# Performance work log

Measured on AMD Instinct MI355X. Metric: run time of the kernel, lower is better.

## Reference

```python
import jax, jax.numpy as jnp
import numpy as np

B, S, D, H = 2, 2048, 1024, 16
DK = D // H


def setup_inputs() -> dict:
    key = jax.random.key(0)
    ks = jax.random.split(key, 9)
    w_scale = 1.0 / np.sqrt(D)  # xavier-ish scale
    return {
        "q": jax.random.normal(ks[0], (B, S, D), dtype=jnp.float32),
        "k": jax.random.normal(ks[1], (B, S, D), dtype=jnp.float32),
        "v": jax.random.normal(ks[2], (B, S, D), dtype=jnp.float32),
        "A": jax.random.uniform(ks[3], (S, S), dtype=jnp.float32),
        "Wq": jax.random.normal(ks[4], (D, D), dtype=jnp.float32) * w_scale,
        "bq": jnp.zeros((D,), jnp.float32),
        "Wk": jax.random.normal(ks[5], (D, D), dtype=jnp.float32) * w_scale,
        "bk": jnp.zeros((D,), jnp.float32),
        "Wv": jax.random.normal(ks[6], (D, D), dtype=jnp.float32) * w_scale,
        "bv": jnp.zeros((D,), jnp.float32),
        "Wo": jax.random.normal(ks[7], (D, D), dtype=jnp.float32) * w_scale,
        "bo": jnp.zeros((D,), jnp.float32),
    }


def _proj(x, W, b):
    # nn.Linear: x @ W^T + b, then split heads -> [B, H, S, DK]
    y = jnp.einsum("bsd,ed->bse", x, W) + b
    return y.reshape(B, S, H, DK).transpose(0, 2, 1, 3)


def reference(q, k, v, A, Wq, bq, Wk, bk, Wv, bv, Wo, bo):
    qh = _proj(q, Wq, bq)  # [B,H,S,DK]
    kh = _proj(k, Wk, bk)
    vh = _proj(v, Wv, bv)
    scale = 1.0 / jnp.sqrt(jnp.asarray(DK, qh.dtype))
    scores = jnp.einsum("bhqd,bhkd->bhqk", qh, kh) * scale  # [B,H,S,S]
    # No softmax: scores multiplied by structural mask A^T (dropout disabled, eval)
    p_attn = scores * A.T
    x = jnp.einsum("bhqk,bhkd->bhqd", p_attn, vh)
    x = x.transpose(0, 2, 1, 3).reshape(B, S, D)
    return jnp.einsum("bsd,ed->bse", x, Wo) + bo
```

## Files before the change

kernel.cpp:

```cpp
#include <hip/hip_runtime.h>

#define SEQ    2048
#define DMODEL 1024
#define NHEAD  16
#define DHEAD  64
#define NBATCH 2

typedef __bf16 bf16x8 __attribute__((ext_vector_type(8)));
typedef float f32x16 __attribute__((ext_vector_type(16)));
typedef float f32x8 __attribute__((ext_vector_type(8)));
typedef unsigned short ushort8v __attribute__((ext_vector_type(8)));
typedef unsigned int uint2v __attribute__((ext_vector_type(2)));
typedef int int4v __attribute__((ext_vector_type(4)));

static __device__ __forceinline__ unsigned short f2b(float f){
  unsigned int u = __builtin_bit_cast(unsigned int, f);
  u += 0x7fffu + ((u>>16)&1u);
  return (unsigned short)(u>>16);
}
static __device__ __forceinline__ float b2f(unsigned short h){
  unsigned int u = ((unsigned int)h)<<16;
  return __builtin_bit_cast(float, u);
}
static __device__ __forceinline__ f32x16 mfma32(bf16x8 a, bf16x8 b, f32x16 c){
  return __builtin_amdgcn_mfma_f32_32x32x16_bf16(a,b,c,0,0,0);
}
static __device__ __forceinline__ ushort8v cvt8(const float* p){
  float4 f0 = *(const float4*)p;
  float4 f1 = *(const float4*)(p+4);
  ushort8v r;
  r[0]=f2b(f0.x); r[1]=f2b(f0.y); r[2]=f2b(f0.z); r[3]=f2b(f0.w);
  r[4]=f2b(f1.x); r[5]=f2b(f1.y); r[6]=f2b(f1.z); r[7]=f2b(f1.w);
  return r;
}
#define GLOAD16(g,l) __builtin_amdgcn_global_load_lds( \
    (const __attribute__((address_space(1))) void*)(g), \
    (__attribute__((address_space(3))) void*)(l), 16, 0, 0)

__global__ __launch_bounds__(256) void cvtXW(
    const float* __restrict__ q, const float* __restrict__ k, const float* __restrict__ v,
    const float* __restrict__ Wq, const float* __restrict__ Wk,
    const float* __restrict__ Wv, const float* __restrict__ Wo,
    unsigned short* __restrict__ Xq, unsigned short* __restrict__ Xk, unsigned short* __restrict__ Xv,
    unsigned short* __restrict__ Wp)
{
  const int z = blockIdx.z;
  const int wave = threadIdx.x>>6, lane = threadIdx.x&63;
  const int l31 = lane&31, hi = lane>>5;
  const float* S;
  unsigned short* dst;
  int g;
  if (z < 3){
    S = (z==0)? q : (z==1)? k : v;
    unsigned short* D = (z==0)? Xq : (z==1)? Xk : Xv;
    g = blockIdx.x;
    dst = D + (size_t)(g*64 + wave*16)*512 + lane*8;
  } else {
    const int wz = blockIdx.x>>5, gg = blockIdx.x&31;
    S = (wz==0)? Wq : (wz==1)? Wk : (wz==2)? Wv : Wo;
    g = gg;
    dst = Wp + (size_t)((wz*32 + gg)*64 + wave*16)*512 + lane*8;
  }
  const float* src = S + (size_t)(g*32 + l31)*DMODEL + 8*hi + 256*wave;
  #pragma unroll
  for (int i=0;i<16;i++)
    *(ushort8v*)(dst + (size_t)i*512) = cvt8(src + 16*i);
}

__global__ __launch_bounds__(256) void cvtA(const float* __restrict__ A,
                                            unsigned short* __restrict__ Am){
  const int tid  = threadIdx.x;
  const int lane = tid&63, l31 = lane&31, hi = lane>>5;
  const int q32  = blockIdx.x;
  const int kt   = blockIdx.y*4 + (tid>>6);
  const int q    = q32*32 + l31;

  unsigned short out8[4][8];
  #pragma unroll
  for (int fi=0; fi<2; fi++){
    #pragma unroll
    for (int mm=0; mm<4; mm++){
      #pragma unroll
      for (int j=0; j<4; j++){
        const int k = kt*64 + 32*fi + 8*mm + 4*hi + j;
        out8[fi*2 + (mm>>1)][(mm&1)*4 + j] = f2b(A[(size_t)k*SEQ + q]);
      }
    }
  }
  unsigned short* dst = Am + ((size_t)(q32*32 + kt)*4)*512 + lane*8;
  #pragma unroll
  for (int w=0; w<4; w++)
    *(ushort8v*)(dst + (size_t)w*512) = *(const ushort8v*)out8[w];
}

__global__ __launch_bounds__(256,3) void proj_qkv(
    const unsigned short* __restrict__ Xq, const unsigned short* __restrict__ Xk, const unsigned short* __restrict__ Xv,
    const unsigned short* __restrict__ Wp,
    const float* __restrict__ bq, const float* __restrict__ bk, const float* __restrict__ bv,
    unsigned short* __restrict__ qh, unsigned short* __restrict__ Kp, unsigned short* __restrict__ Vp)
{
  const int z = blockIdx.z;
  const unsigned short* X = (z==0)? Xq : (z==1)? Xk : Xv;
  const unsigned short* W = Wp + (size_t)z*1048576;
  const float* bias = (z==0)? bq : (z==1)? bk : bv;
  const float alpha = (z==0)? 0.125f : 1.0f;

  const int orig = blockIdx.y*8 + blockIdx.x;
  const int virt = (orig&7)*32 + (orig>>3);
  const int bx = virt&7, by = virt>>3;
  const int mb = by*128, nb = bx*128;

  const int tid = threadIdx.x;
  const int lane = tid&63, wave = tid>>6;
  const int wr = wave>>1, wc = wave&1, l31 = lane&31, hi = lane>>5;
  f32x16 acc[2][2] = {};

  const unsigned short* a0p = X + (size_t)((mb>>5) + 2*wr)*32768 + lane*8;
  const unsigned short* a1p = a0p + 32768;
  const unsigned short* b0p = W + (size_t)((nb>>5) + 2*wc)*32768 + lane*8;
  const unsigned short* b1p = b0p + 32768;

  #pragma unroll 8
  for (int s=0;s<64;s++){
    bf16x8 a0 = *(const bf16x8*)(a0p + (size_t)s*512);
    bf16x8 a1 = *(const bf16x8*)(a1p + (size_t)s*512);
    bf16x8 b0 = *(const bf16x8*)(b0p + (size_t)s*512);
    bf16x8 b1 = *(const bf16x8*)(b1p + (size_t)s*512);
    acc[0][0] = mfma32(a0,b0,acc[0][0]);
    acc[0][1] = mfma32(a0,b1,acc[0][1]);
    acc[1][0] = mfma32(a1,b0,acc[1][0]);
    acc[1][1] = mfma32(a1,b1,acc[1][1]);
  }

  #pragma unroll
  for (int fj=0; fj<2; fj++){
    const int e = nb + 64*wc + 32*fj + l31;
    const float bv_ = bias[e];
    const int hh = e>>6, dk = e&63;
    #pragma unroll
    for (int fi=0; fi<2; fi++){
      #pragma unroll
      for (int r=0;r<16;r++){
        const int i = mb + 64*wr + 32*fi + (r&3) + 8*(r>>2) + 4*hi;
        const int bb = i>>11, ss = i&(SEQ-1);
        const int bhh = bb*NHEAD + hh;
        const unsigned short val = f2b((acc[fi][fj][r] + bv_)*alpha);
        if (z==0){
          qh[((size_t)bhh*SEQ + ss)*DHEAD + dk] = val;
        } else if (z==1){
          const size_t addr = (((size_t)(bhh*64 + (ss>>5))*4 + (dk>>4))*64
                               + ((dk>>3)&1)*32 + (ss&31))*8 + (dk&7);
          Kp[addr] = val;
        } else {
          const size_t addr = ((((size_t)(bhh*32 + (ss>>6))*4 + ((ss>>4)&3))*2
                               + (dk>>5))*64 + ((ss>>3)&1)*32 + (dk&31))*8 + (ss&7);
          Vp[addr] = val;
        }
      }
    }
  }
}

__global__ __launch_bounds__(512,4) void attn(
    const unsigned short* __restrict__ qh, const unsigned short* __restrict__ Kp,
    const unsigned short* __restrict__ Vp, const unsigned short* __restrict__ Am,
    unsigned short* __restrict__ xp)
{
  const int orig = blockIdx.y*16 + blockIdx.x;
  const int xcd = orig&7, within = orig>>3;
  const int bh   = xcd*4 + (within>>4);
  const int qblk = within&15;

  const int tid  = threadIdx.x;
  const int lane = tid&63, wave = tid>>6;
  const int qsub = wave&3, khalf = wave>>2;
  const int l31 = lane&31, hi = lane>>5;

  const int q32  = qblk*4 + qsub;
  const int qrow = q32*32 + l31;
  const unsigned short* qp = qh + ((size_t)bh*SEQ + qrow)*DHEAD;
  bf16x8 Qf[4];
  #pragma unroll
  for (int t=0;t<4;t++) Qf[t] = *(const bf16x8*)(qp + 16*t + 8*hi);

  f32x16 xacc[2] = {};

  const unsigned short* kpb = Kp + (size_t)bh*131072 + lane*8;
  const unsigned short* vpb = Vp + (size_t)bh*131072 + lane*8;
  const unsigned short* apb = Am + (size_t)q32*65536 + lane*8;

  __shared__ float SMEMf[8448];
  unsigned short* smem = (unsigned short*)SMEMf;

  const unsigned short* gsb = ((wave<4)? kpb : vpb);
  const int fo = (wave&3)*2;
  const int dof = ((wave<4)? 0 : 4096) + fo*512;

  ushort8v Aa[2], Ab[2];

  #define STAGE(BUF, KT) { \
    const unsigned short* _g = gsb + (size_t)(KT)*4096 + (size_t)fo*512; \
    GLOAD16(_g,       smem + (BUF)*8192 + dof); \
    GLOAD16(_g + 512, smem + (BUF)*8192 + dof + 512); }

  #define LOADA(DST, KT) { \
    const unsigned short* _ap = apb + (size_t)(KT)*2048 + (size_t)(khalf*2)*512; \
    DST[0] = *(const ushort8v*)(_ap); \
    DST[1] = *(const ushort8v*)(_ap + 512); }

  STAGE(0, 0);  LOADA(Aa, 0);
  STAGE(1, 1);  LOADA(Ab, 1);

  #define ITER(T, BUF, AR, VM, DOSTAGE) { \
    asm volatile("s_waitcnt vmcnt(" VM ")" ::: "memory"); \
    __builtin_amdgcn_sched_barrier(0); \
    __builtin_amdgcn_s_barrier(); \
    __builtin_amdgcn_sched_barrier(0); \
    unsigned int wv[4], xv[4]; \
    { \
      f32x16 sacc = {}; \
      _Pragma("unroll") \
      for (int s=0;s<4;s++){ \
        bf16x8 kf = *(const bf16x8*)(smem + (BUF)*8192 + (khalf*4+s)*512 + lane*8); \
        sacc = mfma32(kf, Qf[s], sacc); \
      } \
      ushort8v a80 = AR[0], a81 = AR[1]; \
      _Pragma("unroll") \
      for (int mm=0; mm<4; mm++){ \
        const int b0 = (mm&1)*4, rb2 = 4*mm; \
        float p0 = sacc[rb2+0]*((mm>>1)? b2f(a81[b0+0]) : b2f(a80[b0+0])); \
        float p1 = sacc[rb2+1]*((mm>>1)? b2f(a81[b0+1]) : b2f(a80[b0+1])); \
        float p2 = sacc[rb2+2]*((mm>>1)? b2f(a81[b0+2]) : b2f(a80[b0+2])); \
        float p3 = sacc[rb2+3]*((mm>>1)? b2f(a81[b0+3]) : b2f(a80[b0+3])); \
        asm("v_cvt_pk_bf16_f32 %0, %1, %2" : "=v"(wv[mm]) : "v"(p0), "v"(p1)); \
        asm("v_cvt_pk_bf16_f32 %0, %1, %2" : "=v"(xv[mm]) : "v"(p2), "v"(p3)); \
      } \
    } \
    __builtin_amdgcn_s_setprio(1); \
    _Pragma("unroll") \
    for (int sl=0; sl<2; sl++){ \
      const int s2 = 2*khalf + sl; \
      uint2v rw = __builtin_amdgcn_permlane32_swap(wv[2*sl], wv[2*sl+1], false, false); \
      uint2v rx = __builtin_amdgcn_permlane32_swap(xv[2*sl], xv[2*sl+1], false, false); \
      int4v av; av.x = (int)rw[0]; av.y = (int)rx[0]; av.z = (int)rw[1]; av.w = (int)rx[1]; \
      bf16x8 pa = __builtin_bit_cast(bf16x8, av); \
      bf16x8 v0 = *(const bf16x8*)(smem + (BUF)*8192 + 4096 + (s2*2+0)*512 + lane*8); \
      bf16x8 v1 = *(const bf16x8*)(smem + (BUF)*8192 + 4096 + (s2*2+1)*512 + lane*8); \
      xacc[0] = mfma32(pa, v0, xacc[0]); \
      xacc[1] = mfma32(pa, v1, xacc[1]); \
    } \
    __builtin_amdgcn_s_setprio(0); \
    __builtin_amdgcn_sched_barrier(0); \
    __builtin_amdgcn_s_barrier(); \
    __builtin_amdgcn_sched_barrier(0); \
    if (DOSTAGE){ \
      STAGE(BUF, (T)+2); \
      LOADA(AR, (T)+2); \
    } }

  #pragma unroll 1
  for (int tt=0; tt<15; tt++){
    const int t0 = 2*tt, t1 = 2*tt+1;
    ITER(t0, 0, Aa, "6", 1);
    ITER(t1, 1, Ab, "6", 1);
  }
  ITER(30, 0, Aa, "6", 0);
  ITER(31, 1, Ab, "0", 0);
  #undef ITER
  #undef STAGE
  #undef LOADA

  float* red = SMEMf;
  __syncthreads();
  if (khalf==1){
    #pragma unroll
    for (int j=0;j<2;j++)
      #pragma unroll
      for (int r=0;r<16;r++)
        red[((qsub*64 + lane)*33) + 16*j + r] = xacc[j][r];
  }
  __syncthreads();
  if (khalf==0){
    #pragma unroll
    for (int j=0;j<2;j++)
      #pragma unroll
      for (int r=0;r<16;r++)
        xacc[j][r] += red[((qsub*64 + lane)*33) + 16*j + r];
    const int b = bh>>4, h = bh&15;
    #pragma unroll
    for (int fj=0; fj<2; fj++){
      const int scol = h*4 + fj*2 + (l31>>4);
      const int lpart = ((l31>>3)&1)*32;
      const int epart = l31&7;
      #pragma unroll
      for (int r=0;r<16;r++){
        const int qq = q32*32 + (r&3) + 8*(r>>2) + 4*hi;
        const int row = b*SEQ + qq;
        const size_t addr = ((size_t)(row>>5)*64 + scol)*512 + (lpart + (row&31))*8 + epart;
        xp[addr] = f2b(xacc[fj][r]);
      }
    }
  }
}

__global__ __launch_bounds__(512,2) void oproj(
    const unsigned short* __restrict__ Xp, const unsigned short* __restrict__ Wop,
    const float* __restrict__ bo, float* __restrict__ out)
{
  const int orig = blockIdx.y*8 + blockIdx.x;
  const int virt = (orig&7)*32 + (orig>>3);
  const int bx = virt&7, by = virt>>3;
  const int mb = by*128, nb = bx*128;

  const int tid = threadIdx.x;
  const int lane = tid&63, wave = tid>>6;
  const int wc = wave&1, wr = (wave>>1)&1, ks = wave>>2;
  const int l31 = lane&31, hi = lane>>5;
  f32x16 acc[2][2] = {};

  const unsigned short* a0p = Xp  + (size_t)((mb>>5) + 2*wr)*32768 + lane*8;
  const unsigned short* a1p = a0p + 32768;
  const unsigned short* b0p = Wop + (size_t)((nb>>5) + 2*wc)*32768 + lane*8;
  const unsigned short* b1p = b0p + 32768;

  const int sbase = ks*32;
  #pragma unroll 8
  for (int s0=0; s0<32; s0++){
    const int s = sbase + s0;
    bf16x8 a0 = *(const bf16x8*)(a0p + (size_t)s*512);
    bf16x8 a1 = *(const bf16x8*)(a1p + (size_t)s*512);
    bf16x8 b0 = *(const bf16x8*)(b0p + (size_t)s*512);
    bf16x8 b1 = *(const bf16x8*)(b1p + (size_t)s*512);
    acc[0][0] = mfma32(a0,b0,acc[0][0]);
    acc[0][1] = mfma32(a0,b1,acc[0][1]);
    acc[1][0] = mfma32(a1,b0,acc[1][0]);
    acc[1][1] = mfma32(a1,b1,acc[1][1]);
  }

  __shared__ float red[4][64][65];
  if (ks==1){
    #pragma unroll
    for (int fi=0; fi<2; fi++)
      #pragma unroll
      for (int fj=0; fj<2; fj++)
        #pragma unroll
        for (int r=0;r<16;r++)
          red[wr*2+wc][lane][(fi*2+fj)*16 + r] = acc[fi][fj][r];
  }
  __syncthreads();
  if (ks==0){
    #pragma unroll
    for (int fi=0; fi<2; fi++)
      #pragma unroll
      for (int fj=0; fj<2; fj++)
        #pragma unroll
        for (int r=0;r<16;r++)
          acc[fi][fj][r] += red[wr*2+wc][lane][(fi*2+fj)*16 + r];
    #pragma unroll
    for (int fj=0; fj<2; fj++){
      const int e = nb + 64*wc + 32*fj + l31;
      const float bv_ = bo[e];
      #pragma unroll
      for (int fi=0; fi<2; fi++){
        #pragma unroll
        for (int r=0;r<16;r++){
          const int i = mb + 64*wr + 32*fi + (r&3) + 8*(r>>2) + 4*hi;
          out[(size_t)i*DMODEL + e] = acc[fi][fj][r] + bv_;
        }
      }
    }
  }
}

extern "C" void kernel_launch(void* const* d_in, const int* in_sizes, int n_in,
                              void* d_out, int out_size, void* d_ws, size_t ws_size,
                              hipStream_t stream)
{
  const float* q  = (const float*)d_in[0];
  const float* k  = (const float*)d_in[1];
  const float* v  = (const float*)d_in[2];
  const float* A  = (const float*)d_in[3];
  const float* Wq = (const float*)d_in[4];
  const float* bq = (const float*)d_in[5];
  const float* Wk = (const float*)d_in[6];
  const float* bk = (const float*)d_in[7];
  const float* Wv = (const float*)d_in[8];
  const float* bv = (const float*)d_in[9];
  const float* Wo = (const float*)d_in[10];
  const float* bo = (const float*)d_in[11];
  float* out = (float*)d_out;

  unsigned short* ws = (unsigned short*)d_ws;
  const size_t NE = (size_t)NBATCH*SEQ*DMODEL;
  unsigned short* qh  = ws;
  unsigned short* Kp  = qh + NE;
  unsigned short* Vp  = Kp + NE;
  unsigned short* xb  = Vp + NE;
  unsigned short* Wp  = xb + NE;
  unsigned short* Xqp = (unsigned short*)d_out;
  unsigned short* Xkp = Xqp + NE;
  unsigned short* Am  = (unsigned short*)d_out;
  unsigned short* Xvp = xb;

  cvtXW<<<dim3(128, 1, 4), 256, 0, stream>>>(q, k, v, Wq, Wk, Wv, Wo,
                                             Xqp, Xkp, Xvp, Wp);
  proj_qkv<<<dim3(8, 32, 3), 256, 0, stream>>>(
      Xqp, Xkp, Xvp, Wp, bq, bk, bv, qh, Kp, Vp);
  cvtA<<<dim3(64, 8), 256, 0, stream>>>(A, Am);
  attn<<<dim3(16, 32), 512, 0, stream>>>(qh, Kp, Vp, Am, xb);
  oproj<<<dim3(8, 32), 512, 0, stream>>>(xb, Wp + (size_t)3*1048576, bo, out);
}
```

Before: 125.9 us.

## Stage QKV projection operand tiles through LDS with cooperative loads

Operand fragments were previously loaded by each wave straight from global memory, so waves sharing a row or column block fetched the same data repeatedly. Now each block loads its A and B tiles cooperatively into shared memory with 16-byte direct-to-LDS loads, and the waves read fragments from LDS. This cuts redundant global and L2 traffic, but adds two barriers per k-step and has no double buffering, so load latency is no longer overlapped with MFMA work.

```diff
diff --git a/kernel.cpp b/kernel.cpp
--- a/kernel.cpp
+++ b/kernel.cpp
@@ -115,21 +115,35 @@
   const int wr = wave>>1, wc = wave&1, l31 = lane&31, hi = lane>>5;
   f32x16 acc[2][2] = {};
 
-  const unsigned short* a0p = X + (size_t)((mb>>5) + 2*wr)*32768 + lane*8;
-  const unsigned short* a1p = a0p + 32768;
-  const unsigned short* b0p = W + (size_t)((nb>>5) + 2*wc)*32768 + lane*8;
-  const unsigned short* b1p = b0p + 32768;
-
-  #pragma unroll 8
-  for (int s=0;s<64;s++){
-    bf16x8 a0 = *(const bf16x8*)(a0p + (size_t)s*512);
-    bf16x8 a1 = *(const bf16x8*)(a1p + (size_t)s*512);
-    bf16x8 b0 = *(const bf16x8*)(b0p + (size_t)s*512);
-    bf16x8 b1 = *(const bf16x8*)(b1p + (size_t)s*512);
-    acc[0][0] = mfma32(a0,b0,acc[0][0]);
-    acc[0][1] = mfma32(a0,b1,acc[0][1]);
-    acc[1][0] = mfma32(a1,b0,acc[1][0]);
-    acc[1][1] = mfma32(a1,b1,acc[1][1]);
+  __shared__ unsigned short SM[16384];
+
+  const unsigned short* gsrc = (wave<2)
+      ? X + (size_t)(mb>>5)*32768 + lane*8
+      : W + (size_t)(nb>>5)*32768 + lane*8;
+  const int cbase = (wave&1)*8;
+  unsigned short* ldst = SM + ((wave<2)? 0 : 8192) + cbase*512 + 0;
+
+  #pragma unroll 1
+  for (int kb=0; kb<16; kb++){
+    #pragma unroll
+    for (int c=0;c<8;c++){
+      const int cc = cbase + c;
+      const int m32 = cc>>2, s0 = cc&3;
+      GLOAD16(gsrc + (size_t)m32*32768 + (size_t)(kb*4+s0)*512, ldst + c*512);
+    }
+    __syncthreads();
+    #pragma unroll
+    for (int s0=0;s0<4;s0++){
+      bf16x8 a0 = *(const bf16x8*)(SM + (8*wr +     s0)*512 + lane*8);
+      bf16x8 a1 = *(const bf16x8*)(SM + (8*wr + 4 + s0)*512 + lane*8);
+      bf16x8 b0 = *(const bf16x8*)(SM + 8192 + (8*wc +     s0)*512 + lane*8);
+      bf16x8 b1 = *(const bf16x8*)(SM + 8192 + (8*wc + 4 + s0)*512 + lane*8);
+      acc[0][0] = mfma32(a0,b0,acc[0][0]);
+      acc[0][1] = mfma32(a0,b1,acc[0][1]);
+      acc[1][0] = mfma32(a1,b0,acc[1][0]);
+      acc[1][1] = mfma32(a1,b1,acc[1][1]);
+    }
+    __syncthreads();
   }
 
   #pragma unroll
```

After: 122.0 us. -3.1%, faster.

## Stage projection GEMM tiles through double-buffered LDS with async global loads

Applied to the files above, without the earlier changes.

Replaces direct per-wave global loads in the QKV projection GEMM with a shared-memory tile staged by a subset of waves using a GLOAD16 direct-to-LDS path. Two buffers are used so the next tile's loads overlap compute on the current one, guarded by vmcnt waits and workgroup barriers. This removes redundant global reads (A and B tiles were loaded separately by each wave pair) and hides load latency. In exchange it adds two barriers per k-step and LDS usage that may limit occupancy.

```diff
diff --git a/kernel.cpp b/kernel.cpp
--- a/kernel.cpp
+++ b/kernel.cpp
@@ -115,22 +115,55 @@
   const int wr = wave>>1, wc = wave&1, l31 = lane&31, hi = lane>>5;
   f32x16 acc[2][2] = {};
 
-  const unsigned short* a0p = X + (size_t)((mb>>5) + 2*wr)*32768 + lane*8;
-  const unsigned short* a1p = a0p + 32768;
-  const unsigned short* b0p = W + (size_t)((nb>>5) + 2*wc)*32768 + lane*8;
-  const unsigned short* b1p = b0p + 32768;
-
-  #pragma unroll 8
-  for (int s=0;s<64;s++){
-    bf16x8 a0 = *(const bf16x8*)(a0p + (size_t)s*512);
-    bf16x8 a1 = *(const bf16x8*)(a1p + (size_t)s*512);
-    bf16x8 b0 = *(const bf16x8*)(b0p + (size_t)s*512);
-    bf16x8 b1 = *(const bf16x8*)(b1p + (size_t)s*512);
-    acc[0][0] = mfma32(a0,b0,acc[0][0]);
-    acc[0][1] = mfma32(a0,b1,acc[0][1]);
-    acc[1][0] = mfma32(a1,b0,acc[1][0]);
-    acc[1][1] = mfma32(a1,b1,acc[1][1]);
-  }
+  __shared__ unsigned short SM[16384];
+
+  const unsigned short* gbase = (wave<2)
+      ? X + (size_t)((mb>>5) + (wave&1)*2)*32768 + lane*8
+      : W + (size_t)((nb>>5) + (wave&1)*2)*32768 + lane*8;
+  unsigned short* lbase = SM + ((wave<2)? 0 : 4096) + (wave&1)*2048;
+
+  #define PSTAGE(BUF, T) { \
+    _Pragma("unroll") \
+    for (int c=0;c<4;c++){ \
+      GLOAD16(gbase + (size_t)(c>>1)*32768 + (size_t)((T)*2 + (c&1))*512, \
+              lbase + (BUF)*8192 + ((c>>1)*2 + (c&1))*512); } }
+
+  #define PCOMP(BUF) { \
+    _Pragma("unroll") \
+    for (int s0=0;s0<2;s0++){ \
+      bf16x8 a0 = *(const bf16x8*)(SM + (BUF)*8192 + (4*wr     + s0)*512 + lane*8); \
+      bf16x8 a1 = *(const bf16x8*)(SM + (BUF)*8192 + (4*wr + 2 + s0)*512 + lane*8); \
+      bf16x8 b0 = *(const bf16x8*)(SM + (BUF)*8192 + 4096 + (4*wc     + s0)*512 + lane*8); \
+      bf16x8 b1 = *(const bf16x8*)(SM + (BUF)*8192 + 4096 + (4*wc + 2 + s0)*512 + lane*8); \
+      acc[0][0] = mfma32(a0,b0,acc[0][0]); \
+      acc[0][1] = mfma32(a0,b1,acc[0][1]); \
+      acc[1][0] = mfma32(a1,b0,acc[1][0]); \
+      acc[1][1] = mfma32(a1,b1,acc[1][1]); } }
+
+  #define PITER(T, BUF, VM, DOSTAGE) { \
+    asm volatile("s_waitcnt vmcnt(" VM ")" ::: "memory"); \
+    __builtin_amdgcn_sched_barrier(0); \
+    __builtin_amdgcn_s_barrier(); \
+    __builtin_amdgcn_sched_barrier(0); \
+    PCOMP(BUF); \
+    __builtin_amdgcn_sched_barrier(0); \
+    __builtin_amdgcn_s_barrier(); \
+    __builtin_amdgcn_sched_barrier(0); \
+    if (DOSTAGE) PSTAGE(BUF, (T)+2); }
+
+  PSTAGE(0, 0);
+  PSTAGE(1, 1);
+
+  #pragma unroll 1
+  for (int tt=0; tt<15; tt++){
+    PITER(2*tt,   0, "4", 1);
+    PITER(2*tt+1, 1, "4", 1);
+  }
+  PITER(30, 0, "4", 0);
+  PITER(31, 1, "0", 0);
+  #undef PITER
+  #undef PCOMP
+  #undef PSTAGE
 
   #pragma unroll
   for (int fj=0; fj<2; fj++){
```

Result: faster. 122.1 us (-3.0%).
